# Performance work log

Measured on AMD Instinct MI355X. Metric: run time of the kernel, lower is better.

The kernel has to match this reference:

```python
import jax, jax.numpy as jnp
import numpy as np

BS = 8  # DCT block size


def _dct_basis():
    x = np.arange(BS)
    u = np.arange(BS)
    M = 0.5 * np.cos((2 * x[None, :] + 1) * u[:, None] * np.pi / 16)
    M[0, :] *= 1.0 / np.sqrt(2.0)
    # Separable 2-D basis: coeff[u, v, x, y] = M[u, x] * M[v, y]
    return jnp.asarray(np.einsum('ux,vy->uvxy', M, M), jnp.float32)


_Q_LUM = np.array([
    [16, 11, 10, 16, 24, 40, 51, 61],
    [12, 12, 14, 19, 26, 58, 60, 55],
    [14, 13, 16, 24, 40, 57, 69, 56],
    [14, 17, 22, 29, 51, 87, 80, 62],
    [18, 22, 37, 56, 68, 109, 103, 77],
    [24, 35, 55, 64, 81, 104, 113, 92],
    [49, 64, 78, 87, 103, 121, 120, 101],
    [72, 92, 95, 98, 112, 100, 103, 99]], dtype=np.float32)

_Q_CHROM = np.array([
    [17, 18, 24, 47, 99, 99, 99, 99],
    [18, 21, 26, 66, 99, 99, 99, 99],
    [24, 26, 56, 99, 99, 99, 99, 99],
    [47, 66, 99, 99, 99, 99, 99, 99],
    [99, 99, 99, 99, 99, 99, 99, 99],
    [99, 99, 99, 99, 99, 99, 99, 99],
    [99, 99, 99, 99, 99, 99, 99, 99],
    [99, 99, 99, 99, 99, 99, 99, 99]], dtype=np.float32)


def setup_inputs() -> dict:
    key = jax.random.key(0)
    image = jax.random.uniform(key, (16, 3, 512, 512), dtype=jnp.float32)
    rgb2yuv = jnp.array([[0.299, 0.587, 0.114],
                         [-0.1687, -0.3313, 0.5],
                         [0.5, -0.4187, -0.0813]], jnp.float32)
    yuv2rgb = jnp.array([[1.0, 0.0, 1.402],
                         [1.0, -0.34414, -0.71414],
                         [1.0, 1.772, 0.0]], jnp.float32)
    return {
        'image': image,
        'rgb2yuv': rgb2yuv,
        'yuv2rgb': yuv2rgb,
        'dct_coeff': _dct_basis(),          # (8,8,8,8)
        'q_lum': jnp.asarray(_Q_LUM),       # (8,8)
        'q_chrom': jnp.asarray(_Q_CHROM),   # (8,8)
    }


def _compress(x, C, Q):
    # x: (b, c, H, W) with H, W multiples of 8; C: (8,8,8,8); Q: (8,8)
    b, c, H, W = x.shape
    nh, nw = H // BS, W // BS
    x = x * 255.0 - 128.0
    # tile into 8x8 blocks: (b, c, nh, nw, 8, 8)
    blk = x.reshape(b, c, nh, BS, nw, BS).transpose(0, 1, 2, 4, 3, 5)
    # forward block DCT: out[u,v] = sum_{x,y} C[u,v,x,y] * blk[x,y]
    d = jnp.einsum('uvxy,bcnmxy->bcnmuv', C, blk)
    # quantize / dequantize (Q broadcasts over the last two (u, v) dims)
    d = jnp.round(d / Q) * Q
    # inverse block DCT (transpose of the orthonormal basis)
    r = jnp.einsum('xyuv,bcnmuv->bcnmxy', C, d)
    img = r.transpose(0, 1, 2, 4, 3, 5).reshape(b, c, H, W)
    return (img + 128.0) / 255.0


def reference(image, rgb2yuv, yuv2rgb, dct_coeff, q_lum, q_chrom):
    yuv = jnp.einsum('ij,bjhw->bihw', rgb2yuv, image)
    y = _compress(yuv[:, 0:1], dct_coeff, q_lum)
    uv = _compress(yuv[:, 1:], dct_coeff, q_chrom)
    out = jnp.einsum('ij,bjhw->bihw', yuv2rgb, jnp.concatenate([y, uv], axis=1))
    return out
```

## Files before the change

kernel.cpp:

```cpp
#include <hip/hip_runtime.h>
#include <math.h>

#define CSTRIDE (512 * 512)

__device__ __forceinline__ float chain_dot64_nofma(const float* __restrict__ c,
                                                   const float* __restrict__ v)
{
#pragma clang fp contract(off)
    float s = 0.0f;
#pragma unroll
    for (int q = 0; q < 64; ++q) s = s + c[q] * v[q];
    return s;
}

__global__ __launch_bounds__(256, 3)
void jpeg_kernel(const float* __restrict__ img,
                 const float* __restrict__ rgb2yuv,
                 const float* __restrict__ yuv2rgb,
                 const float* __restrict__ dctC,
                 const float* __restrict__ qlum,
                 const float* __restrict__ qchrom,
                 float* __restrict__ out)
{
#pragma clang fp contract(off)
    __shared__ float V[3][4096];

    const int tid  = threadIdx.x;
    const int lane = tid & 63;
    const int wv   = tid >> 6;
    const int p0u  = __builtin_amdgcn_readfirstlane(wv * 16);

    const int b  = blockIdx.x >> 6;
    const int y0 = (blockIdx.x & 63) << 3;
    const size_t base0 = (size_t)b * 3 * CSTRIDE + (size_t)y0 * 512;

    const float r00 = rgb2yuv[0], r01 = rgb2yuv[1], r02 = rgb2yuv[2];
    const float r10 = rgb2yuv[3], r11 = rgb2yuv[4], r12 = rgb2yuv[5];
    const float r20 = rgb2yuv[6], r21 = rgb2yuv[7], r22 = rgb2yuv[8];

#pragma unroll
    for (int i = 0; i < 4; ++i) {
        const size_t f4 = 4 * (size_t)(tid + 256 * i);
        const float4 R4 = *(const float4*)(img + base0 + f4);
        const float4 G4 = *(const float4*)(img + base0 + CSTRIDE + f4);
        const float4 B4 = *(const float4*)(img + base0 + 2 * CSTRIDE + f4);
        const float* rp = (const float*)&R4;
        const float* gp = (const float*)&G4;
        const float* bp = (const float*)&B4;
#pragma unroll
        for (int jj = 0; jj < 4; ++jj) {
            const int flat = 4 * (tid + 256 * i) + jj;
            const int w = flat & 511, x = flat >> 9;
            const int idx = ((x << 3) + (w & 7)) * 64 + (w >> 3);
            const float r_ = rp[jj], g_ = gp[jj], b_ = bp[jj];
            float t;
            t = (r00 * r_ + r01 * g_) + r02 * b_;  V[0][idx] = t * 255.0f - 128.0f;
            t = (r10 * r_ + r11 * g_) + r12 * b_;  V[1][idx] = t * 255.0f - 128.0f;
            t = (r20 * r_ + r21 * g_) + r22 * b_;  V[2][idx] = t * 255.0f - 128.0f;
        }
    }
    __syncthreads();

    const int xb = __builtin_amdgcn_readfirstlane(wv * 2);
    float mrow[2][8];
#pragma unroll
    for (int k = 0; k < 2; ++k)
#pragma unroll
        for (int u = 0; u < 8; ++u)
            mrow[k][u] = dctC[(size_t)(xb + k) * 512 + u * 8] * 2.82842712474619f;

    const float MT[8][8] = {
        { 0.353553391f,  0.353553391f,  0.353553391f,  0.353553391f,  0.353553391f,  0.353553391f,  0.353553391f,  0.353553391f},
        { 0.490392640f,  0.415734806f,  0.277785117f,  0.097545161f, -0.097545161f, -0.277785117f, -0.415734806f, -0.490392640f},
        { 0.461939766f,  0.191341716f, -0.191341716f, -0.461939766f, -0.461939766f, -0.191341716f,  0.191341716f,  0.461939766f},
        { 0.415734806f, -0.097545161f, -0.490392640f, -0.277785117f,  0.277785117f,  0.490392640f,  0.097545161f, -0.415734806f},
        { 0.353553391f, -0.353553391f, -0.353553391f,  0.353553391f,  0.353553391f, -0.353553391f, -0.353553391f,  0.353553391f},
        { 0.277785117f, -0.490392640f,  0.097545161f,  0.415734806f, -0.415734806f, -0.097545161f,  0.490392640f, -0.277785117f},
        { 0.191341716f, -0.461939766f,  0.461939766f, -0.191341716f, -0.191341716f,  0.461939766f, -0.461939766f,  0.191341716f},
        { 0.097545161f, -0.277785117f,  0.415734806f, -0.490392640f,  0.490392640f, -0.415734806f,  0.277785117f, -0.097545161f}};

    for (int c = 0; c < 3; ++c) {
        float* Vc = V[c];

        float v[64];
#pragma unroll
        for (int q = 0; q < 64; ++q) v[q] = Vc[q * 64 + lane];
        __syncthreads();

        const float* qtab = (c == 0) ? qlum : qchrom;
        for (int j = 0; j < 16; ++j) {
            const float* Crow = dctC + (size_t)(p0u + j) * 64;
            const float d  = chain_dot64_nofma(Crow, v);
            const float qv = qtab[p0u + j];
            const float dq = rintf(d / qv) * qv;
            Vc[(p0u + j) * 64 + lane] = dq;
        }
        __syncthreads();

        float t[64];
#pragma unroll
        for (int u = 0; u < 8; ++u) {
            float du[8];
#pragma unroll
            for (int q = 0; q < 8; ++q) du[q] = Vc[(u * 8 + q) * 64 + lane];
#pragma unroll
            for (int y = 0; y < 8; ++y) {
                float s = MT[y][0] * du[0];
#pragma unroll
                for (int q = 1; q < 8; ++q) s = fmaf(MT[y][q], du[q], s);
                t[u * 8 + y] = s;
            }
        }
        __syncthreads();

#pragma unroll
        for (int j = 0; j < 16; ++j) {
            const int k = j >> 3, y = j & 7;
            float s = mrow[k][0] * t[y];
#pragma unroll
            for (int u = 1; u < 8; ++u) s = fmaf(mrow[k][u], t[u * 8 + y], s);
            Vc[(p0u + j) * 64 + lane] = s;
        }
    }
    __syncthreads();

    const float s255 = 1.0f / 255.0f;
    const float c00 = yuv2rgb[0] * s255, c01 = yuv2rgb[1] * s255, c02 = yuv2rgb[2] * s255;
    const float c10 = yuv2rgb[3] * s255, c11 = yuv2rgb[4] * s255, c12 = yuv2rgb[5] * s255;
    const float c20 = yuv2rgb[6] * s255, c21 = yuv2rgb[7] * s255, c22 = yuv2rgb[8] * s255;
    const float k0 = (yuv2rgb[0] + yuv2rgb[1] + yuv2rgb[2]) * (128.0f / 255.0f);
    const float k1 = (yuv2rgb[3] + yuv2rgb[4] + yuv2rgb[5]) * (128.0f / 255.0f);
    const float k2 = (yuv2rgb[6] + yuv2rgb[7] + yuv2rgb[8]) * (128.0f / 255.0f);

#pragma unroll
    for (int i = 0; i < 4; ++i) {
        float4 o0, o1, o2;
        float* q0 = (float*)&o0; float* q1 = (float*)&o1; float* q2 = (float*)&o2;
#pragma unroll
        for (int jj = 0; jj < 4; ++jj) {
            const int flat = 4 * (tid + 256 * i) + jj;
            const int w = flat & 511, x = flat >> 9;
            const int cell = ((x << 3) + (w & 7)) * 64 + (w >> 3);
            const float Yv = V[0][cell], Uv = V[1][cell], Wv = V[2][cell];
            q0[jj] = fmaf(c00, Yv, fmaf(c01, Uv, fmaf(c02, Wv, k0)));
            q1[jj] = fmaf(c10, Yv, fmaf(c11, Uv, fmaf(c12, Wv, k1)));
            q2[jj] = fmaf(c20, Yv, fmaf(c21, Uv, fmaf(c22, Wv, k2)));
        }
        const size_t f4 = 4 * (size_t)(tid + 256 * i);
        *(float4*)(out + base0 + f4)                = o0;
        *(float4*)(out + base0 + CSTRIDE + f4)      = o1;
        *(float4*)(out + base0 + 2 * CSTRIDE + f4)  = o2;
    }
}

extern "C" void kernel_launch(void* const* d_in, const int* in_sizes, int n_in,
                              void* d_out, int out_size, void* d_ws, size_t ws_size,
                              hipStream_t stream) {
    const float* img = (const float*)d_in[0];
    const float* r2y = (const float*)d_in[1];
    const float* y2r = (const float*)d_in[2];
    const float* C   = (const float*)d_in[3];
    const float* ql  = (const float*)d_in[4];
    const float* qc  = (const float*)d_in[5];
    float* o = (float*)d_out;

    jpeg_kernel<<<dim3(16 * 64), dim3(256), 0, stream>>>(img, r2y, y2r, C, ql, qc, o);
}
```

Baseline: 158.5 us.

## Cut shared memory to two planes by re-reading the image for the V channel

```diff
diff --git a/kernel.cpp b/kernel.cpp
--- a/kernel.cpp
+++ b/kernel.cpp
@@ -13,7 +13,7 @@
     return s;
 }
 
-__global__ __launch_bounds__(256, 3)
+__global__ __launch_bounds__(256, 4)
 void jpeg_kernel(const float* __restrict__ img,
                  const float* __restrict__ rgb2yuv,
                  const float* __restrict__ yuv2rgb,
@@ -23,7 +23,8 @@
                  float* __restrict__ out)
 {
 #pragma clang fp contract(off)
-    __shared__ float V[3][4096];
+    __shared__ float A[4096];
+    __shared__ float B[4096];
 
     const int tid  = threadIdx.x;
     const int lane = tid & 63;
@@ -54,9 +55,8 @@
             const int idx = ((x << 3) + (w & 7)) * 64 + (w >> 3);
             const float r_ = rp[jj], g_ = gp[jj], b_ = bp[jj];
             float t;
-            t = (r00 * r_ + r01 * g_) + r02 * b_;  V[0][idx] = t * 255.0f - 128.0f;
-            t = (r10 * r_ + r11 * g_) + r12 * b_;  V[1][idx] = t * 255.0f - 128.0f;
-            t = (r20 * r_ + r21 * g_) + r22 * b_;  V[2][idx] = t * 255.0f - 128.0f;
+            t = (r00 * r_ + r01 * g_) + r02 * b_;  A[idx] = t * 255.0f - 128.0f;
+            t = (r10 * r_ + r11 * g_) + r12 * b_;  B[idx] = t * 255.0f - 128.0f;
         }
     }
     __syncthreads();
@@ -79,15 +79,12 @@
         { 0.191341716f, -0.461939766f,  0.461939766f, -0.191341716f, -0.191341716f,  0.461939766f, -0.461939766f,  0.191341716f},
         { 0.097545161f, -0.277785117f,  0.415734806f, -0.490392640f,  0.490392640f, -0.415734806f,  0.277785117f, -0.097545161f}};
 
-    for (int c = 0; c < 3; ++c) {
-        float* Vc = V[c];
-
+    auto proc = [&](float* Vc, const float* qtab) {
         float v[64];
 #pragma unroll
         for (int q = 0; q < 64; ++q) v[q] = Vc[q * 64 + lane];
         __syncthreads();
 
-        const float* qtab = (c == 0) ? qlum : qchrom;
         for (int j = 0; j < 16; ++j) {
             const float* Crow = dctC + (size_t)(p0u + j) * 64;
             const float d  = chain_dot64_nofma(Crow, v);
@@ -121,7 +118,45 @@
             for (int u = 1; u < 8; ++u) s = fmaf(mrow[k][u], t[u * 8 + y], s);
             Vc[(p0u + j) * 64 + lane] = s;
         }
-    }
+    };
+
+    proc(A, qlum);
+    __syncthreads();
+
+    float recY[16];
+#pragma unroll
+    for (int i = 0; i < 4; ++i) {
+#pragma unroll
+        for (int jj = 0; jj < 4; ++jj) {
+            const int flat = 4 * (tid + 256 * i) + jj;
+            const int w = flat & 511, x = flat >> 9;
+            recY[i * 4 + jj] = A[((x << 3) + (w & 7)) * 64 + (w >> 3)];
+        }
+    }
+    __syncthreads();
+
+#pragma unroll
+    for (int i = 0; i < 4; ++i) {
+        const size_t f4 = 4 * (size_t)(tid + 256 * i);
+        const float4 R4 = *(const float4*)(img + base0 + f4);
+        const float4 G4 = *(const float4*)(img + base0 + CSTRIDE + f4);
+        const float4 B4 = *(const float4*)(img + base0 + 2 * CSTRIDE + f4);
+        const float* rp = (const float*)&R4;
+        const float* gp = (const float*)&G4;
+        const float* bp = (const float*)&B4;
+#pragma unroll
+        for (int jj = 0; jj < 4; ++jj) {
+            const int flat = 4 * (tid + 256 * i) + jj;
+            const int w = flat & 511, x = flat >> 9;
+            const int idx = ((x << 3) + (w & 7)) * 64 + (w >> 3);
+            const float tW = (r20 * rp[jj] + r21 * gp[jj]) + r22 * bp[jj];
+            A[idx] = tW * 255.0f - 128.0f;
+        }
+    }
+    __syncthreads();
+
+    proc(A, qchrom);
+    proc(B, qchrom);
     __syncthreads();
 
     const float s255 = 1.0f / 255.0f;
@@ -141,7 +176,9 @@
             const int flat = 4 * (tid + 256 * i) + jj;
             const int w = flat & 511, x = flat >> 9;
             const int cell = ((x << 3) + (w & 7)) * 64 + (w >> 3);
-            const float Yv = V[0][cell], Uv = V[1][cell], Wv = V[2][cell];
+            const float Yv = recY[i * 4 + jj];
+            const float Uv = B[cell];
+            const float Wv = A[cell];
             q0[jj] = fmaf(c00, Yv, fmaf(c01, Uv, fmaf(c02, Wv, k0)));
             q1[jj] = fmaf(c10, Yv, fmaf(c11, Uv, fmaf(c12, Wv, k1)));
             q2[jj] = fmaf(c20, Yv, fmaf(c21, Uv, fmaf(c22, Wv, k2)));
```

New measurement: 200.0 us. +26.2%, slower.

## Store quantized DCT indices as shorts and fold color conversion into inverse DCT

Applied to the files above, without the earlier changes.

```diff
diff --git a/kernel.cpp b/kernel.cpp
--- a/kernel.cpp
+++ b/kernel.cpp
@@ -13,7 +13,7 @@
     return s;
 }
 
-__global__ __launch_bounds__(256, 3)
+__global__ __launch_bounds__(256)
 void jpeg_kernel(const float* __restrict__ img,
                  const float* __restrict__ rgb2yuv,
                  const float* __restrict__ yuv2rgb,
@@ -23,7 +23,9 @@
                  float* __restrict__ out)
 {
 #pragma clang fp contract(off)
-    __shared__ float V[3][4096];
+    __shared__ float A[4096];
+    __shared__ int   NYU[4096];
+    __shared__ short NW[4096];
 
     const int tid  = threadIdx.x;
     const int lane = tid & 63;
@@ -33,33 +35,6 @@
     const int b  = blockIdx.x >> 6;
     const int y0 = (blockIdx.x & 63) << 3;
     const size_t base0 = (size_t)b * 3 * CSTRIDE + (size_t)y0 * 512;
-
-    const float r00 = rgb2yuv[0], r01 = rgb2yuv[1], r02 = rgb2yuv[2];
-    const float r10 = rgb2yuv[3], r11 = rgb2yuv[4], r12 = rgb2yuv[5];
-    const float r20 = rgb2yuv[6], r21 = rgb2yuv[7], r22 = rgb2yuv[8];
-
-#pragma unroll
-    for (int i = 0; i < 4; ++i) {
-        const size_t f4 = 4 * (size_t)(tid + 256 * i);
-        const float4 R4 = *(const float4*)(img + base0 + f4);
-        const float4 G4 = *(const float4*)(img + base0 + CSTRIDE + f4);
-        const float4 B4 = *(const float4*)(img + base0 + 2 * CSTRIDE + f4);
-        const float* rp = (const float*)&R4;
-        const float* gp = (const float*)&G4;
-        const float* bp = (const float*)&B4;
-#pragma unroll
-        for (int jj = 0; jj < 4; ++jj) {
-            const int flat = 4 * (tid + 256 * i) + jj;
-            const int w = flat & 511, x = flat >> 9;
-            const int idx = ((x << 3) + (w & 7)) * 64 + (w >> 3);
-            const float r_ = rp[jj], g_ = gp[jj], b_ = bp[jj];
-            float t;
-            t = (r00 * r_ + r01 * g_) + r02 * b_;  V[0][idx] = t * 255.0f - 128.0f;
-            t = (r10 * r_ + r11 * g_) + r12 * b_;  V[1][idx] = t * 255.0f - 128.0f;
-            t = (r20 * r_ + r21 * g_) + r22 * b_;  V[2][idx] = t * 255.0f - 128.0f;
-        }
-    }
-    __syncthreads();
 
     const int xb = __builtin_amdgcn_readfirstlane(wv * 2);
     float mrow[2][8];
@@ -79,30 +54,73 @@
         { 0.191341716f, -0.461939766f,  0.461939766f, -0.191341716f, -0.191341716f,  0.461939766f, -0.461939766f,  0.191341716f},
         { 0.097545161f, -0.277785117f,  0.415734806f, -0.490392640f,  0.490392640f, -0.415734806f,  0.277785117f, -0.097545161f}};
 
-    for (int c = 0; c < 3; ++c) {
-        float* Vc = V[c];
+    for (int ch = 0; ch < 3; ++ch) {
+        const float m0 = rgb2yuv[3 * ch + 0];
+        const float m1 = rgb2yuv[3 * ch + 1];
+        const float m2 = rgb2yuv[3 * ch + 2];
+
+#pragma unroll
+        for (int i = 0; i < 4; ++i) {
+            const size_t f4 = 4 * (size_t)(tid + 256 * i);
+            const float4 R4 = *(const float4*)(img + base0 + f4);
+            const float4 G4 = *(const float4*)(img + base0 + CSTRIDE + f4);
+            const float4 B4 = *(const float4*)(img + base0 + 2 * CSTRIDE + f4);
+            const float* rp = (const float*)&R4;
+            const float* gp = (const float*)&G4;
+            const float* bp = (const float*)&B4;
+#pragma unroll
+            for (int jj = 0; jj < 4; ++jj) {
+                const int flat = 4 * (tid + 256 * i) + jj;
+                const int w = flat & 511, x = flat >> 9;
+                const int idx = ((x << 3) + (w & 7)) * 64 + (w >> 3);
+                const float t = (m0 * rp[jj] + m1 * gp[jj]) + m2 * bp[jj];
+                A[idx] = t * 255.0f - 128.0f;
+            }
+        }
+        __syncthreads();
 
         float v[64];
 #pragma unroll
-        for (int q = 0; q < 64; ++q) v[q] = Vc[q * 64 + lane];
-        __syncthreads();
+        for (int q = 0; q < 64; ++q) v[q] = A[q * 64 + lane];
 
-        const float* qtab = (c == 0) ? qlum : qchrom;
+        const float* qtab = (ch == 0) ? qlum : qchrom;
+        short* nyus = (short*)NYU;
         for (int j = 0; j < 16; ++j) {
             const float* Crow = dctC + (size_t)(p0u + j) * 64;
             const float d  = chain_dot64_nofma(Crow, v);
             const float qv = qtab[p0u + j];
-            const float dq = rintf(d / qv) * qv;
-            Vc[(p0u + j) * 64 + lane] = dq;
+            const short n  = (short)(int)rintf(d / qv);
+            const int cell = (p0u + j) * 64 + lane;
+            if (ch == 0)      nyus[2 * cell]     = n;
+            else if (ch == 1) nyus[2 * cell + 1] = n;
+            else              NW[cell]           = n;
         }
         __syncthreads();
+    }
+
+    const float s255 = 1.0f / 255.0f;
+
+    for (int oc = 0; oc < 3; ++oc) {
+        const float m0 = yuv2rgb[3 * oc + 0];
+        const float m1 = yuv2rgb[3 * oc + 1];
+        const float m2 = yuv2rgb[3 * oc + 2];
+        const float koc = (m0 + m1 + m2) * (128.0f / 255.0f);
 
         float t[64];
 #pragma unroll
         for (int u = 0; u < 8; ++u) {
             float du[8];
 #pragma unroll
-            for (int q = 0; q < 8; ++q) du[q] = Vc[(u * 8 + q) * 64 + lane];
+            for (int q = 0; q < 8; ++q) {
+                const int cell = (u * 8 + q) * 64 + lane;
+                const int pk = NYU[cell];
+                const float nY = (float)(short)(pk & 0xFFFF);
+                const float nU = (float)(short)(pk >> 16);
+                const float nWv = (float)NW[cell];
+                const float ql = qlum[u * 8 + q];
+                const float qc = qchrom[u * 8 + q];
+                du[q] = fmaf(m0, nY * ql, fmaf(m1, nU * qc, m2 * (nWv * qc)));
+            }
 #pragma unroll
             for (int y = 0; y < 8; ++y) {
                 float s = MT[y][0] * du[0];
@@ -119,37 +137,24 @@
             float s = mrow[k][0] * t[y];
 #pragma unroll
             for (int u = 1; u < 8; ++u) s = fmaf(mrow[k][u], t[u * 8 + y], s);
-            Vc[(p0u + j) * 64 + lane] = s;
+            A[(p0u + j) * 64 + lane] = s;
         }
-    }
-    __syncthreads();
-
-    const float s255 = 1.0f / 255.0f;
-    const float c00 = yuv2rgb[0] * s255, c01 = yuv2rgb[1] * s255, c02 = yuv2rgb[2] * s255;
-    const float c10 = yuv2rgb[3] * s255, c11 = yuv2rgb[4] * s255, c12 = yuv2rgb[5] * s255;
-    const float c20 = yuv2rgb[6] * s255, c21 = yuv2rgb[7] * s255, c22 = yuv2rgb[8] * s255;
-    const float k0 = (yuv2rgb[0] + yuv2rgb[1] + yuv2rgb[2]) * (128.0f / 255.0f);
-    const float k1 = (yuv2rgb[3] + yuv2rgb[4] + yuv2rgb[5]) * (128.0f / 255.0f);
-    const float k2 = (yuv2rgb[6] + yuv2rgb[7] + yuv2rgb[8]) * (128.0f / 255.0f);
+        __syncthreads();
 
 #pragma unroll
-    for (int i = 0; i < 4; ++i) {
-        float4 o0, o1, o2;
-        float* q0 = (float*)&o0; float* q1 = (float*)&o1; float* q2 = (float*)&o2;
+        for (int i = 0; i < 4; ++i) {
+            float4 o;
+            float* qo = (float*)&o;
 #pragma unroll
-        for (int jj = 0; jj < 4; ++jj) {
-            const int flat = 4 * (tid + 256 * i) + jj;
-            const int w = flat & 511, x = flat >> 9;
-            const int cell = ((x << 3) + (w & 7)) * 64 + (w >> 3);
-            const float Yv = V[0][cell], Uv = V[1][cell], Wv = V[2][cell];
-            q0[jj] = fmaf(c00, Yv, fmaf(c01, Uv, fmaf(c02, Wv, k0)));
-            q1[jj] = fmaf(c10, Yv, fmaf(c11, Uv, fmaf(c12, Wv, k1)));
-            q2[jj] = fmaf(c20, Yv, fmaf(c21, Uv, fmaf(c22, Wv, k2)));
+            for (int jj = 0; jj < 4; ++jj) {
+                const int flat = 4 * (tid + 256 * i) + jj;
+                const int w = flat & 511, x = flat >> 9;
+                const int cell = ((x << 3) + (w & 7)) * 64 + (w >> 3);
+                qo[jj] = fmaf(A[cell], s255, koc);
+            }
+            const size_t f4 = 4 * (size_t)(tid + 256 * i);
+            *(float4*)(out + base0 + (size_t)oc * CSTRIDE + f4) = o;
         }
-        const size_t f4 = 4 * (size_t)(tid + 256 * i);
-        *(float4*)(out + base0 + f4)                = o0;
-        *(float4*)(out + base0 + CSTRIDE + f4)      = o1;
-        *(float4*)(out + base0 + 2 * CSTRIDE + f4)  = o2;
     }
 }
 
```

Result: slower. 175.8 us (+10.9%).

## Fuse YUV-to-RGB into inverse DCT with register accumulators and direct stores

Applied to the files above, without the earlier changes.

```diff
diff --git a/kernel.cpp b/kernel.cpp
--- a/kernel.cpp
+++ b/kernel.cpp
@@ -79,8 +79,23 @@
         { 0.191341716f, -0.461939766f,  0.461939766f, -0.191341716f, -0.191341716f,  0.461939766f, -0.461939766f,  0.191341716f},
         { 0.097545161f, -0.277785117f,  0.415734806f, -0.490392640f,  0.490392640f, -0.415734806f,  0.277785117f, -0.097545161f}};
 
+    const float s255 = 1.0f / 255.0f;
+    const float c00 = yuv2rgb[0] * s255, c01 = yuv2rgb[1] * s255, c02 = yuv2rgb[2] * s255;
+    const float c10 = yuv2rgb[3] * s255, c11 = yuv2rgb[4] * s255, c12 = yuv2rgb[5] * s255;
+    const float c20 = yuv2rgb[6] * s255, c21 = yuv2rgb[7] * s255, c22 = yuv2rgb[8] * s255;
+    const float k0 = (yuv2rgb[0] + yuv2rgb[1] + yuv2rgb[2]) * (128.0f / 255.0f);
+    const float k1 = (yuv2rgb[3] + yuv2rgb[4] + yuv2rgb[5]) * (128.0f / 255.0f);
+    const float k2 = (yuv2rgb[6] + yuv2rgb[7] + yuv2rgb[8]) * (128.0f / 255.0f);
+
+    float accR[16], accG[16], accB[16];
+#pragma unroll
+    for (int j = 0; j < 16; ++j) { accR[j] = k0; accG[j] = k1; accB[j] = k2; }
+
     for (int c = 0; c < 3; ++c) {
         float* Vc = V[c];
+        const float cR = (c == 0) ? c00 : ((c == 1) ? c01 : c02);
+        const float cG = (c == 0) ? c10 : ((c == 1) ? c11 : c12);
+        const float cB = (c == 0) ? c20 : ((c == 1) ? c21 : c22);
 
         float v[64];
 #pragma unroll
@@ -111,7 +126,6 @@
                 t[u * 8 + y] = s;
             }
         }
-        __syncthreads();
 
 #pragma unroll
         for (int j = 0; j < 16; ++j) {
@@ -119,37 +133,28 @@
             float s = mrow[k][0] * t[y];
 #pragma unroll
             for (int u = 1; u < 8; ++u) s = fmaf(mrow[k][u], t[u * 8 + y], s);
-            Vc[(p0u + j) * 64 + lane] = s;
+            accR[j] = fmaf(cR, s, accR[j]);
+            accG[j] = fmaf(cG, s, accG[j]);
+            accB[j] = fmaf(cB, s, accB[j]);
         }
     }
-    __syncthreads();
-
-    const float s255 = 1.0f / 255.0f;
-    const float c00 = yuv2rgb[0] * s255, c01 = yuv2rgb[1] * s255, c02 = yuv2rgb[2] * s255;
-    const float c10 = yuv2rgb[3] * s255, c11 = yuv2rgb[4] * s255, c12 = yuv2rgb[5] * s255;
-    const float c20 = yuv2rgb[6] * s255, c21 = yuv2rgb[7] * s255, c22 = yuv2rgb[8] * s255;
-    const float k0 = (yuv2rgb[0] + yuv2rgb[1] + yuv2rgb[2]) * (128.0f / 255.0f);
-    const float k1 = (yuv2rgb[3] + yuv2rgb[4] + yuv2rgb[5]) * (128.0f / 255.0f);
-    const float k2 = (yuv2rgb[6] + yuv2rgb[7] + yuv2rgb[8]) * (128.0f / 255.0f);
 
 #pragma unroll
-    for (int i = 0; i < 4; ++i) {
-        float4 o0, o1, o2;
-        float* q0 = (float*)&o0; float* q1 = (float*)&o1; float* q2 = (float*)&o2;
-#pragma unroll
-        for (int jj = 0; jj < 4; ++jj) {
-            const int flat = 4 * (tid + 256 * i) + jj;
-            const int w = flat & 511, x = flat >> 9;
-            const int cell = ((x << 3) + (w & 7)) * 64 + (w >> 3);
-            const float Yv = V[0][cell], Uv = V[1][cell], Wv = V[2][cell];
-            q0[jj] = fmaf(c00, Yv, fmaf(c01, Uv, fmaf(c02, Wv, k0)));
-            q1[jj] = fmaf(c10, Yv, fmaf(c11, Uv, fmaf(c12, Wv, k1)));
-            q2[jj] = fmaf(c20, Yv, fmaf(c21, Uv, fmaf(c22, Wv, k2)));
-        }
-        const size_t f4 = 4 * (size_t)(tid + 256 * i);
-        *(float4*)(out + base0 + f4)                = o0;
-        *(float4*)(out + base0 + CSTRIDE + f4)      = o1;
-        *(float4*)(out + base0 + 2 * CSTRIDE + f4)  = o2;
+    for (int g = 0; g < 2; ++g) {
+        const size_t rb = base0 + (size_t)(2 * wv + g) * 512 + 8 * (size_t)lane;
+        float4 o;
+        o.x = accR[g*8+0]; o.y = accR[g*8+1]; o.z = accR[g*8+2]; o.w = accR[g*8+3];
+        *(float4*)(out + rb) = o;
+        o.x = accR[g*8+4]; o.y = accR[g*8+5]; o.z = accR[g*8+6]; o.w = accR[g*8+7];
+        *(float4*)(out + rb + 4) = o;
+        o.x = accG[g*8+0]; o.y = accG[g*8+1]; o.z = accG[g*8+2]; o.w = accG[g*8+3];
+        *(float4*)(out + CSTRIDE + rb) = o;
+        o.x = accG[g*8+4]; o.y = accG[g*8+5]; o.z = accG[g*8+6]; o.w = accG[g*8+7];
+        *(float4*)(out + CSTRIDE + rb + 4) = o;
+        o.x = accB[g*8+0]; o.y = accB[g*8+1]; o.z = accB[g*8+2]; o.w = accB[g*8+3];
+        *(float4*)(out + 2 * CSTRIDE + rb) = o;
+        o.x = accB[g*8+4]; o.y = accB[g*8+5]; o.z = accB[g*8+6]; o.w = accB[g*8+7];
+        *(float4*)(out + 2 * CSTRIDE + rb + 4) = o;
     }
 }
 
```

Result: slower. 243.1 us (+53.4%).
